# Performance work log

Hardware: AMD Instinct MI355X
Metric: run time of the kernel (lower is better)

The kernel has to match this reference:

```python
import jax, jax.numpy as jnp
import numpy as np

N_NODES = 8192
N_EDGES = 262144
D_IN, D_HID, D_OUT = 128, 64, 32
DROP_P = 0.1


def _glorot(key, shape):
    lim = (6.0 / (shape[0] + shape[1])) ** 0.5
    return jax.random.uniform(key, shape, jnp.float32, -lim, lim)


def setup_inputs() -> dict:
    key = jax.random.key(0)
    ks = jax.random.split(key, 8)
    x = jax.random.normal(ks[0], (N_NODES, D_IN), jnp.float32)
    edge_index = jax.random.randint(ks[1], (2, N_EDGES), 0, N_NODES, jnp.int64)
    # GCNConv params: linear weight [in, out] (x @ W) + bias, 3 layers
    W0 = _glorot(ks[2], (D_IN, D_HID)); b0 = jnp.zeros((D_HID,), jnp.float32)
    W1 = _glorot(ks[3], (D_HID, D_HID)); b1 = jnp.zeros((D_HID,), jnp.float32)
    W2 = _glorot(ks[4], (D_HID, D_OUT)); b2 = jnp.zeros((D_OUT,), jnp.float32)
    return {"x": x, "W0": W0, "b0": b0, "W1": W1, "b1": b1,
            "W2": W2, "b2": b2, "edge_index": edge_index}


def _gcn(adj, x, W, b):
    # PyG GCNConv: add self-loops, symmetric normalization D^-1/2 (A+I) D^-1/2
    n = adj.shape[0]
    a = adj + jnp.eye(n, dtype=adj.dtype)
    dinv = jax.lax.rsqrt(a.sum(axis=1))  # deg >= 1 due to self-loop
    a = dinv[:, None] * a * dinv[None, :]
    return a @ (x @ W) + b


def reference(x, W0, b0, W1, b1, W2, b2, edge_index):
    n = x.shape[0]
    # binary dense adjacency of the ORIGINAL graph (to_dense_adj analogue)
    adj0 = jnp.zeros((n, n), x.dtype).at[edge_index[0], edge_index[1]].set(1.0)
    rng = jax.random.key(42)
    params = [(W0, b0), (W1, b1), (W2, b2)]
    adj = adj0
    z = x
    for i, (W, b) in enumerate(params):
        z = jax.nn.relu(_gcn(adj, z, W, b))
        kd, kb = jax.random.split(jax.random.fold_in(rng, i))
        keep = jax.random.bernoulli(kd, 1.0 - DROP_P, z.shape)
        z = jnp.where(keep, z / (1.0 - DROP_P), 0.0)  # Dropout(0.1), train mode
        if i < len(params) - 1:  # last resample never affects the output
            prob = jax.nn.sigmoid(z @ z.T)                      # [N, N]
            sample = (jax.random.uniform(kb, prob.shape) < prob).astype(z.dtype)
            adj = adj0 * sample  # Bernoulli-masked original edges
    return z
```

## Files before the change

### kernel.cpp

```cpp
#include <hip/hip_runtime.h>
#include <stdint.h>
#include <math.h>

#define NN 8192
#define NE 262144
#define CAP 96

struct TFKey { uint32_t a, b; };

__host__ __device__ static inline void tf2x32(uint32_t k0, uint32_t k1,
                                              uint32_t x0, uint32_t x1,
                                              uint32_t* o0, uint32_t* o1) {
  uint32_t ks2 = k0 ^ k1 ^ 0x1BD11BDAu;
#define TF_ROT(x, r) (((x) << (r)) | ((x) >> (32 - (r))))
#define TF_R(r) { x0 += x1; x1 = TF_ROT(x1, r); x1 ^= x0; }
  x0 += k0; x1 += k1;
  TF_R(13) TF_R(15) TF_R(26) TF_R(6)
  x0 += k1;  x1 += ks2 + 1u;
  TF_R(17) TF_R(29) TF_R(16) TF_R(24)
  x0 += ks2; x1 += k0 + 2u;
  TF_R(13) TF_R(15) TF_R(26) TF_R(6)
  x0 += k0;  x1 += k1 + 3u;
  TF_R(17) TF_R(29) TF_R(16) TF_R(24)
  x0 += k1;  x1 += ks2 + 4u;
  TF_R(13) TF_R(15) TF_R(26) TF_R(6)
  x0 += ks2; x1 += k0 + 5u;
  *o0 = x0; *o1 = x1;
#undef TF_R
#undef TF_ROT
}

__device__ static inline float tf_uniform(TFKey k, uint32_t n) {
  uint32_t o0, o1;
  tf2x32(k.a, k.b, 0u, n, &o0, &o1);
  uint32_t bits = o0 ^ o1;
  return __uint_as_float((bits >> 9) | 0x3f800000u) - 1.0f;
}


template<int K, int N>
__device__ __forceinline__ void gemm_elem(const float* __restrict__ A,
                                          const float* __restrict__ Wb,
                                          float* __restrict__ H, int t) {
  int i = t / N, c = t % N;
  double a0 = 0.0, a1 = 0.0;
#pragma unroll 8
  for (int k = 0; k < K; k += 2) {
    a0 += (double)A[(size_t)i * K + k] * (double)Wb[(size_t)k * N + c];
    a1 += (double)A[(size_t)i * K + k + 1] * (double)Wb[(size_t)(k + 1) * N + c];
  }
  H[t] = (float)(a0 + a1);
}

template<int D>
__device__ __forceinline__ void agg_row(const uint16_t* __restrict__ cols,
                                        const uint32_t* __restrict__ deg,
                                        const uint8_t* __restrict__ mask,
                                        const float* __restrict__ h,
                                        const float* __restrict__ dinv,
                                        const float* __restrict__ bias,
                                        TFKey kd, float* __restrict__ zout,
                                        int i, int lane) {
  bool act = lane < D;
  float di = dinv[i];
  uint32_t du = deg[i];
  uint32_t d = du < (uint32_t)CAP ? du : (uint32_t)CAP;
  const uint16_t* cr = cols + (size_t)i * CAP;
  const uint8_t* mr = mask ? mask + (size_t)i * CAP : (const uint8_t*)nullptr;
  double a0 = 0.0, a1 = 0.0;
  uint32_t s = 0;
  for (; s + 1 < d; s += 2) {
    int j0 = cr[s], j1 = cr[s + 1];
    bool m0 = !mr || mr[s], m1 = !mr || mr[s + 1];
    if (act) {
      if (m0) { float c0 = di * dinv[j0]; a0 += (double)c0 * (double)h[(size_t)j0 * D + lane]; }
      if (m1) { float c1 = di * dinv[j1]; a1 += (double)c1 * (double)h[(size_t)j1 * D + lane]; }
    }
  }
  if (s < d && (!mr || mr[s]) && act) {
    int j = cr[s];
    float c = di * dinv[j];
    a0 += (double)c * (double)h[(size_t)j * D + lane];
  }
  if (act) {
    double acc = a0 + a1;
    float cI = di * di;
    acc += (double)cI * (double)h[(size_t)i * D + lane];
    float sv = (float)acc;
    float pre = fmaxf(sv + bias[lane], 0.0f);
    float u = tf_uniform(kd, (uint32_t)(i * D + lane));
    zout[(size_t)i * D + lane] = (u < 0.9f) ? (pre / 0.9f) : 0.0f;
  }
}

__device__ __forceinline__ void sample_row(const uint16_t* __restrict__ cols,
                                           const uint32_t* __restrict__ deg,
                                           const float* __restrict__ z,
                                           TFKey kb, uint8_t* __restrict__ mask,
                                           float* __restrict__ dinv,
                                           int i, int lane) {
  int g = lane >> 4, l = lane & 15;
  float4 zi = *(const float4*)(z + (size_t)i * 64 + 4 * l);
  uint32_t du = deg[i];
  uint32_t d = du < (uint32_t)CAP ? du : (uint32_t)CAP;
  const uint16_t* cr = cols + (size_t)i * CAP;
  uint8_t* mr = mask + (size_t)i * CAP;
  int cnt = 0;
  for (uint32_t base = 0; base < d; base += 4) {
    uint32_t s = base + (uint32_t)g;
    bool on = s < d;
    int j = 0;
    if (on) j = cr[s];
    float4 b = *(const float4*)(z + (size_t)j * 64 + 4 * l);
    double p = (double)zi.x * (double)b.x + (double)zi.y * (double)b.y
             + (double)zi.z * (double)b.z + (double)zi.w * (double)b.w;
    p += __shfl_xor(p, 1, 64);
    p += __shfl_xor(p, 2, 64);
    p += __shfl_xor(p, 4, 64);
    p += __shfl_xor(p, 8, 64);
    if (l == 0 && on) {
      float dot32 = (float)p;
      float prob = (float)(1.0 / (1.0 + exp(-(double)dot32)));
      float u = tf_uniform(kb, (uint32_t)((i << 13) | j));
      uint8_t m = (u < prob) ? 1u : 0u;
      mr[s] = m;
      cnt += m;
    }
  }
  cnt += __shfl_xor(cnt, 16, 64);
  cnt += __shfl_xor(cnt, 32, 64);
  if (lane == 0) dinv[i] = (float)(1.0 / sqrt((double)(cnt + 1)));
}


__global__ __launch_bounds__(256) void k_init0(const int* __restrict__ e,
                                               uint32_t* __restrict__ deg,
                                               uint32_t* __restrict__ flag) {
  uint32_t t = blockIdx.x * 256 + threadIdx.x;
  deg[t] = 0u;
  if (blockIdx.x == 0) {
    const unsigned long long* p = (const unsigned long long*)e;
    bool bad = false;
    for (int q = 0; q < 8; ++q)
      bad |= (p[threadIdx.x * 8 + q] >= 8192ull);
    __shared__ uint32_t sh[4];
    unsigned long long b = __ballot(bad);
    if ((threadIdx.x & 63) == 0) sh[threadIdx.x >> 6] = (b != 0ull) ? 1u : 0u;
    __syncthreads();
    if (threadIdx.x == 0) flag[0] = sh[0] | sh[1] | sh[2] | sh[3];
  }
}

__global__ __launch_bounds__(256) void k_g0s(const float* __restrict__ x,
                                             const float* __restrict__ W0,
                                             float* __restrict__ h,
                                             const int* __restrict__ e,
                                             const uint32_t* __restrict__ flag,
                                             uint32_t* __restrict__ deg,
                                             uint16_t* __restrict__ cols) {
  constexpr int GB0 = NN * 64 / 256;
  if (blockIdx.x < GB0) {
    gemm_elem<128, 64>(x, W0, h, blockIdx.x * 256 + threadIdx.x);
  } else {
    int ed = (blockIdx.x - GB0) * 256 + threadIdx.x;
    int r, c;
    if (*flag) { r = e[ed]; c = e[ed + NE]; }
    else { const long long* p = (const long long*)e; r = (int)p[ed]; c = (int)p[ed + NE]; }
    uint32_t s = atomicAdd(&deg[r], 1u);
    if (s < CAP) cols[(size_t)r * CAP + s] = (uint16_t)c;
  }
}

__global__ __launch_bounds__(256) void k_dedup(uint16_t* __restrict__ cols,
                                               uint32_t* __restrict__ deg,
                                               float* __restrict__ dinv) {
  __shared__ uint32_t bits[4][256];
  __shared__ uint32_t ucnt[4];
  int lane = threadIdx.x & 63;
  int wv = threadIdx.x >> 6;
  int i = blockIdx.x * 4 + wv;
  ((uint4*)bits[wv])[lane] = make_uint4(0u, 0u, 0u, 0u);
  if (lane == 0) ucnt[wv] = 0u;
  __syncthreads();
  uint32_t draw = deg[i];
  if (draw > (uint32_t)CAP) draw = (uint32_t)CAP;
  uint16_t* cr = cols + (size_t)i * CAP;
  uint32_t c0 = 0xFFFFFFFFu, c1 = 0xFFFFFFFFu;
  if ((uint32_t)lane < draw) c0 = cr[lane];
  if ((uint32_t)(lane + 64) < draw) c1 = cr[lane + 64];
  if (c0 != 0xFFFFFFFFu) {
    uint32_t bit = 1u << (c0 & 31);
    uint32_t old = atomicOr(&bits[wv][c0 >> 5], bit);
    if (!(old & bit)) { uint32_t p = atomicAdd(&ucnt[wv], 1u); cr[p] = (uint16_t)c0; }
  }
  if (c1 != 0xFFFFFFFFu) {
    uint32_t bit = 1u << (c1 & 31);
    uint32_t old = atomicOr(&bits[wv][c1 >> 5], bit);
    if (!(old & bit)) { uint32_t p = atomicAdd(&ucnt[wv], 1u); cr[p] = (uint16_t)c1; }
  }
  if (lane == 0) {
    uint32_t u = ucnt[wv];
    deg[i] = u;
    dinv[i] = (float)(1.0 / sqrt((double)(u + 1u)));
  }
}

template<int D>
__global__ __launch_bounds__(256) void k_agg(const uint16_t* __restrict__ cols,
                                             const uint32_t* __restrict__ deg,
                                             const uint8_t* __restrict__ mask,
                                             const float* __restrict__ h,
                                             const float* __restrict__ dinv,
                                             const float* __restrict__ bias,
                                             TFKey kd, float* __restrict__ zout) {
  int lane = threadIdx.x & 63;
  int i = blockIdx.x * 4 + (threadIdx.x >> 6);
  agg_row<D>(cols, deg, mask, h, dinv, bias, kd, zout, i, lane);
}

template<int K, int N>
__global__ __launch_bounds__(256) void k_sg(const float* __restrict__ z,
                                            const float* __restrict__ Wb,
                                            float* __restrict__ h,
                                            const uint16_t* __restrict__ cols,
                                            const uint32_t* __restrict__ deg,
                                            TFKey kb,
                                            uint8_t* __restrict__ mask,
                                            float* __restrict__ dinv) {
  constexpr int GB = NN * N / 256;
  if (blockIdx.x < GB) {
    gemm_elem<K, N>(z, Wb, h, blockIdx.x * 256 + threadIdx.x);
  } else {
    int lane = threadIdx.x & 63;
    int i = (blockIdx.x - GB) * 4 + (threadIdx.x >> 6);
    sample_row(cols, deg, z, kb, mask, dinv, i, lane);
  }
}


extern "C" void kernel_launch(void* const* d_in, const int* in_sizes, int n_in,
                              void* d_out, int out_size, void* d_ws, size_t ws_size,
                              hipStream_t stream) {
  (void)in_sizes; (void)n_in; (void)out_size; (void)ws_size;
  const float* x  = (const float*)d_in[0];
  const float* W0 = (const float*)d_in[1];
  const float* b0 = (const float*)d_in[2];
  const float* W1 = (const float*)d_in[3];
  const float* b1 = (const float*)d_in[4];
  const float* W2 = (const float*)d_in[5];
  const float* b2 = (const float*)d_in[6];
  const int* ei = (const int*)d_in[7];
  float* out = (float*)d_out;

  uint8_t* base = (uint8_t*)d_ws;
  float* h        = (float*)(base);
  float* z        = (float*)(base + 2097152);
  uint32_t* deg   = (uint32_t*)(base + 4194304);
  uint16_t* cols  = (uint16_t*)(base + 4194304 + 32768);
  uint8_t*  mask  = (uint8_t*)(base + 4194304 + 32768 + 1572864);
  float*    dinv  = (float*)(base + 4194304 + 32768 + 1572864 + 786432);
  uint32_t* flag  = (uint32_t*)(base + 4194304 + 32768 + 1572864 + 786432 + 32768);

  TFKey kd[3], kb[3];
  for (uint32_t i = 0; i < 3; ++i) {
    uint32_t la, lb;
    tf2x32(0u, 42u, 0u, i, &la, &lb);
    tf2x32(la, lb, 0u, 0u, &kd[i].a, &kd[i].b);
    tf2x32(la, lb, 0u, 1u, &kb[i].a, &kb[i].b);
  }

  k_init0<<<NN / 256, 256, 0, stream>>>(ei, deg, flag);
  k_g0s  <<<NN * 64 / 256 + NE / 256, 256, 0, stream>>>(x, W0, h, ei, flag, deg, cols);
  k_dedup<<<NN / 4, 256, 0, stream>>>(cols, deg, dinv);
  k_agg<64><<<NN / 4, 256, 0, stream>>>(cols, deg, nullptr, h, dinv, b0, kd[0], z);
  k_sg<64, 64><<<NN * 64 / 256 + NN / 4, 256, 0, stream>>>(z, W1, h, cols, deg, kb[0], mask, dinv);
  k_agg<64><<<NN / 4, 256, 0, stream>>>(cols, deg, mask, h, dinv, b1, kd[1], z);
  k_sg<64, 32><<<NN * 32 / 256 + NN / 4, 256, 0, stream>>>(z, W2, h, cols, deg, kb[1], mask, dinv);
  k_agg<32><<<NN / 4, 256, 0, stream>>>(cols, deg, mask, h, dinv, b2, kd[2], out);
}
```

Measured before the change: 219.4 us.

## Deduplicate edges with a global dense bitmap during build, dropping the dedup kernel

Edge insertion now first sets a bit in an 8 MB dense adjacency bitmap and only appends the column when the bit was previously unset, so duplicates are removed at insertion time. This removes the separate dedup kernel. The first aggregation now computes degree normalisation on the fly from deg instead of reading a dinv array. The first-layer GEMM also reads its input row with float4 loads. The cost is zeroing 8 MB in the init kernel and extra global atomics on the bitmap.

```diff
diff --git a/kernel.cpp b/kernel.cpp
--- a/kernel.cpp
+++ b/kernel.cpp
@@ -4,6 +4,7 @@
 
 #define NN 8192
 #define NE 262144
+#define WPR 256
 #define CAP 96
 
 struct TFKey { uint32_t a, b; };
@@ -43,16 +44,21 @@
                                           const float* __restrict__ Wb,
                                           float* __restrict__ H, int t) {
   int i = t / N, c = t % N;
+  const float4* Arow = (const float4*)(A + (size_t)i * K);
   double a0 = 0.0, a1 = 0.0;
-#pragma unroll 8
-  for (int k = 0; k < K; k += 2) {
-    a0 += (double)A[(size_t)i * K + k] * (double)Wb[(size_t)k * N + c];
-    a1 += (double)A[(size_t)i * K + k + 1] * (double)Wb[(size_t)(k + 1) * N + c];
+#pragma unroll 4
+  for (int k4 = 0; k4 < K / 4; ++k4) {
+    float4 av = Arow[k4];
+    int k = k4 * 4;
+    a0 += (double)av.x * (double)Wb[(size_t)k * N + c];
+    a1 += (double)av.y * (double)Wb[(size_t)(k + 1) * N + c];
+    a0 += (double)av.z * (double)Wb[(size_t)(k + 2) * N + c];
+    a1 += (double)av.w * (double)Wb[(size_t)(k + 3) * N + c];
   }
   H[t] = (float)(a0 + a1);
 }
 
-template<int D>
+template<int D, bool DEG0>
 __device__ __forceinline__ void agg_row(const uint16_t* __restrict__ cols,
                                         const uint32_t* __restrict__ deg,
                                         const uint8_t* __restrict__ mask,
@@ -62,24 +68,33 @@
                                         TFKey kd, float* __restrict__ zout,
                                         int i, int lane) {
   bool act = lane < D;
-  float di = dinv[i];
   uint32_t du = deg[i];
+  float di = DEG0 ? (float)(1.0 / sqrt((double)(du + 1u))) : dinv[i];
   uint32_t d = du < (uint32_t)CAP ? du : (uint32_t)CAP;
   const uint16_t* cr = cols + (size_t)i * CAP;
-  const uint8_t* mr = mask ? mask + (size_t)i * CAP : (const uint8_t*)nullptr;
+  const uint8_t* mr = (!DEG0 && mask) ? mask + (size_t)i * CAP : (const uint8_t*)nullptr;
   double a0 = 0.0, a1 = 0.0;
   uint32_t s = 0;
   for (; s + 1 < d; s += 2) {
     int j0 = cr[s], j1 = cr[s + 1];
-    bool m0 = !mr || mr[s], m1 = !mr || mr[s + 1];
+    bool m0 = DEG0 || !mr || mr[s], m1 = DEG0 || !mr || mr[s + 1];
     if (act) {
-      if (m0) { float c0 = di * dinv[j0]; a0 += (double)c0 * (double)h[(size_t)j0 * D + lane]; }
-      if (m1) { float c1 = di * dinv[j1]; a1 += (double)c1 * (double)h[(size_t)j1 * D + lane]; }
+      if (m0) {
+        float dj0 = DEG0 ? (float)(1.0 / sqrt((double)(deg[j0] + 1u))) : dinv[j0];
+        float c0 = di * dj0;
+        a0 += (double)c0 * (double)h[(size_t)j0 * D + lane];
+      }
+      if (m1) {
+        float dj1 = DEG0 ? (float)(1.0 / sqrt((double)(deg[j1] + 1u))) : dinv[j1];
+        float c1 = di * dj1;
+        a1 += (double)c1 * (double)h[(size_t)j1 * D + lane];
+      }
     }
   }
-  if (s < d && (!mr || mr[s]) && act) {
+  if (s < d && (DEG0 || !mr || mr[s]) && act) {
     int j = cr[s];
-    float c = di * dinv[j];
+    float dj = DEG0 ? (float)(1.0 / sqrt((double)(deg[j] + 1u))) : dinv[j];
+    float c = di * dj;
     a0 += (double)c * (double)h[(size_t)j * D + lane];
   }
   if (act) {
@@ -133,11 +148,13 @@
 }
 
 
-__global__ __launch_bounds__(256) void k_init0(const int* __restrict__ e,
-                                               uint32_t* __restrict__ deg,
-                                               uint32_t* __restrict__ flag) {
+__global__ __launch_bounds__(256) void k_init(const int* __restrict__ e,
+                                              uint32_t* __restrict__ dense,
+                                              uint32_t* __restrict__ deg,
+                                              uint32_t* __restrict__ flag) {
   uint32_t t = blockIdx.x * 256 + threadIdx.x;
-  deg[t] = 0u;
+  ((uint4*)dense)[t] = make_uint4(0u, 0u, 0u, 0u);
+  if (t < NN) deg[t] = 0u;
   if (blockIdx.x == 0) {
     const unsigned long long* p = (const unsigned long long*)e;
     bool bad = false;
@@ -151,13 +168,14 @@
   }
 }
 
-__global__ __launch_bounds__(256) void k_g0s(const float* __restrict__ x,
-                                             const float* __restrict__ W0,
-                                             float* __restrict__ h,
-                                             const int* __restrict__ e,
-                                             const uint32_t* __restrict__ flag,
-                                             uint32_t* __restrict__ deg,
-                                             uint16_t* __restrict__ cols) {
+__global__ __launch_bounds__(256) void k_gb(const float* __restrict__ x,
+                                            const float* __restrict__ W0,
+                                            float* __restrict__ h,
+                                            const int* __restrict__ e,
+                                            const uint32_t* __restrict__ flag,
+                                            uint32_t* __restrict__ dense,
+                                            uint32_t* __restrict__ deg,
+                                            uint16_t* __restrict__ cols) {
   constexpr int GB0 = NN * 64 / 256;
   if (blockIdx.x < GB0) {
     gemm_elem<128, 64>(x, W0, h, blockIdx.x * 256 + threadIdx.x);
@@ -166,46 +184,16 @@
     int r, c;
     if (*flag) { r = e[ed]; c = e[ed + NE]; }
     else { const long long* p = (const long long*)e; r = (int)p[ed]; c = (int)p[ed + NE]; }
-    uint32_t s = atomicAdd(&deg[r], 1u);
-    if (s < CAP) cols[(size_t)r * CAP + s] = (uint16_t)c;
-  }
-}
-
-__global__ __launch_bounds__(256) void k_dedup(uint16_t* __restrict__ cols,
-                                               uint32_t* __restrict__ deg,
-                                               float* __restrict__ dinv) {
-  __shared__ uint32_t bits[4][256];
-  __shared__ uint32_t ucnt[4];
-  int lane = threadIdx.x & 63;
-  int wv = threadIdx.x >> 6;
-  int i = blockIdx.x * 4 + wv;
-  ((uint4*)bits[wv])[lane] = make_uint4(0u, 0u, 0u, 0u);
-  if (lane == 0) ucnt[wv] = 0u;
-  __syncthreads();
-  uint32_t draw = deg[i];
-  if (draw > (uint32_t)CAP) draw = (uint32_t)CAP;
-  uint16_t* cr = cols + (size_t)i * CAP;
-  uint32_t c0 = 0xFFFFFFFFu, c1 = 0xFFFFFFFFu;
-  if ((uint32_t)lane < draw) c0 = cr[lane];
-  if ((uint32_t)(lane + 64) < draw) c1 = cr[lane + 64];
-  if (c0 != 0xFFFFFFFFu) {
-    uint32_t bit = 1u << (c0 & 31);
-    uint32_t old = atomicOr(&bits[wv][c0 >> 5], bit);
-    if (!(old & bit)) { uint32_t p = atomicAdd(&ucnt[wv], 1u); cr[p] = (uint16_t)c0; }
-  }
-  if (c1 != 0xFFFFFFFFu) {
-    uint32_t bit = 1u << (c1 & 31);
-    uint32_t old = atomicOr(&bits[wv][c1 >> 5], bit);
-    if (!(old & bit)) { uint32_t p = atomicAdd(&ucnt[wv], 1u); cr[p] = (uint16_t)c1; }
-  }
-  if (lane == 0) {
-    uint32_t u = ucnt[wv];
-    deg[i] = u;
-    dinv[i] = (float)(1.0 / sqrt((double)(u + 1u)));
-  }
-}
-
-template<int D>
+    uint32_t bit = 1u << (c & 31);
+    uint32_t old = atomicOr(&dense[(size_t)r * WPR + (c >> 5)], bit);
+    if (!(old & bit)) {
+      uint32_t s = atomicAdd(&deg[r], 1u);
+      if (s < CAP) cols[(size_t)r * CAP + s] = (uint16_t)c;
+    }
+  }
+}
+
+template<int D, bool DEG0>
 __global__ __launch_bounds__(256) void k_agg(const uint16_t* __restrict__ cols,
                                              const uint32_t* __restrict__ deg,
                                              const uint8_t* __restrict__ mask,
@@ -215,7 +203,7 @@
                                              TFKey kd, float* __restrict__ zout) {
   int lane = threadIdx.x & 63;
   int i = blockIdx.x * 4 + (threadIdx.x >> 6);
-  agg_row<D>(cols, deg, mask, h, dinv, bias, kd, zout, i, lane);
+  agg_row<D, DEG0>(cols, deg, mask, h, dinv, bias, kd, zout, i, lane);
 }
 
 template<int K, int N>
@@ -253,13 +241,14 @@
   float* out = (float*)d_out;
 
   uint8_t* base = (uint8_t*)d_ws;
-  float* h        = (float*)(base);
-  float* z        = (float*)(base + 2097152);
-  uint32_t* deg   = (uint32_t*)(base + 4194304);
-  uint16_t* cols  = (uint16_t*)(base + 4194304 + 32768);
-  uint8_t*  mask  = (uint8_t*)(base + 4194304 + 32768 + 1572864);
-  float*    dinv  = (float*)(base + 4194304 + 32768 + 1572864 + 786432);
-  uint32_t* flag  = (uint32_t*)(base + 4194304 + 32768 + 1572864 + 786432 + 32768);
+  uint32_t* dense = (uint32_t*)(base);
+  float* h        = (float*)(base + 8388608);
+  float* z        = (float*)(base + 10485760);
+  uint32_t* deg   = (uint32_t*)(base + 12582912);
+  uint16_t* cols  = (uint16_t*)(base + 12582912 + 32768);
+  uint8_t*  mask  = (uint8_t*)(base + 12582912 + 32768 + 1572864);
+  float*    dinv  = (float*)(base + 12582912 + 32768 + 1572864 + 786432);
+  uint32_t* flag  = (uint32_t*)(base + 12582912 + 32768 + 1572864 + 786432 + 32768);
 
   TFKey kd[3], kb[3];
   for (uint32_t i = 0; i < 3; ++i) {
@@ -269,12 +258,11 @@
     tf2x32(la, lb, 0u, 1u, &kb[i].a, &kb[i].b);
   }
 
-  k_init0<<<NN / 256, 256, 0, stream>>>(ei, deg, flag);
-  k_g0s  <<<NN * 64 / 256 + NE / 256, 256, 0, stream>>>(x, W0, h, ei, flag, deg, cols);
-  k_dedup<<<NN / 4, 256, 0, stream>>>(cols, deg, dinv);
-  k_agg<64><<<NN / 4, 256, 0, stream>>>(cols, deg, nullptr, h, dinv, b0, kd[0], z);
+  k_init<<<NN * WPR / (4 * 256), 256, 0, stream>>>(ei, dense, deg, flag);
+  k_gb  <<<NN * 64 / 256 + NE / 256, 256, 0, stream>>>(x, W0, h, ei, flag, dense, deg, cols);
+  k_agg<64, true><<<NN / 4, 256, 0, stream>>>(cols, deg, nullptr, h, dinv, b0, kd[0], z);
   k_sg<64, 64><<<NN * 64 / 256 + NN / 4, 256, 0, stream>>>(z, W1, h, cols, deg, kb[0], mask, dinv);
-  k_agg<64><<<NN / 4, 256, 0, stream>>>(cols, deg, mask, h, dinv, b1, kd[1], z);
+  k_agg<64, false><<<NN / 4, 256, 0, stream>>>(cols, deg, mask, h, dinv, b1, kd[1], z);
   k_sg<64, 32><<<NN * 32 / 256 + NN / 4, 256, 0, stream>>>(z, W2, h, cols, deg, kb[1], mask, dinv);
-  k_agg<32><<<NN / 4, 256, 0, stream>>>(cols, deg, mask, h, dinv, b2, kd[2], out);
-}
+  k_agg<32, false><<<NN / 4, 256, 0, stream>>>(cols, deg, mask, h, dinv, b2, kd[2], out);
+}
```

Result: slower. 237.3 us (+8.2%).
